# Kernel tuning notes

Hardware: AMD Instinct MI355X
Metric: run time of the kernel (lower is better)

Reference implementation:

```python
import jax, jax.numpy as jnp
import numpy as np

NEG_SLOPE = 0.2
EPS = 1e-16


def gat_conv(x, edge_index, W, att_src, att_dst, bias, heads, out_ch, concat):
    """PyG GATConv (eval mode, add_self_loops=True).
    x: [N, F_in], edge_index: [2, E] with row0=src(j), row1=dst(i).
    W: [F_in, heads*out_ch], att_src/att_dst: [heads, out_ch], bias: [heads*out_ch] or [out_ch].
    """
    N = x.shape[0]
    loop = jnp.arange(N, dtype=edge_index.dtype)
    src = jnp.concatenate([edge_index[0], loop])
    dst = jnp.concatenate([edge_index[1], loop])

    h = (x @ W).reshape(N, heads, out_ch)                 # [N, H, C]
    a_src = jnp.sum(h * att_src[None], axis=-1)           # [N, H]
    a_dst = jnp.sum(h * att_dst[None], axis=-1)           # [N, H]

    alpha = jax.nn.leaky_relu(a_src[src] + a_dst[dst], NEG_SLOPE)  # [E, H]
    # segment softmax over incoming edges of each destination node
    m = jax.ops.segment_max(alpha, dst, num_segments=N)   # [N, H]
    e = jnp.exp(alpha - m[dst])                           # [E, H]
    s = jax.ops.segment_sum(e, dst, num_segments=N)       # [N, H]
    alpha = e / (s[dst] + EPS)                            # [E, H]

    out = jax.ops.segment_sum(h[src] * alpha[:, :, None], dst, num_segments=N)  # [N, H, C]
    if concat:
        out = out.reshape(N, heads * out_ch)
    else:
        out = out.mean(axis=1)
    return out + bias


def setup_inputs() -> dict:
    key = jax.random.key(0)
    ks = jax.random.split(key, 12)
    N, E, F_in, C = 100000, 1600000, 512, 16
    H1, O1 = 8, 8
    hid = H1 * O1  # 64
    sc1 = 1.0 / np.sqrt(F_in)
    sc2 = 1.0 / np.sqrt(hid)
    return {
        "x": jax.random.normal(ks[0], (N, F_in), jnp.float32),
        "edge_index": jax.random.randint(ks[1], (2, E), 0, N, jnp.int64),
        "W1": jax.random.normal(ks[2], (F_in, hid), jnp.float32) * sc1,
        "att_src1": jax.random.normal(ks[3], (H1, O1), jnp.float32) * sc2,
        "att_dst1": jax.random.normal(ks[4], (H1, O1), jnp.float32) * sc2,
        "bias1": jnp.zeros((hid,), jnp.float32),
        "W2": jax.random.normal(ks[5], (hid, C), jnp.float32) * sc2,
        "att_src2": jax.random.normal(ks[6], (1, C), jnp.float32) * 0.25,
        "att_dst2": jax.random.normal(ks[7], (1, C), jnp.float32) * 0.25,
        "bias2": jnp.zeros((C,), jnp.float32),
    }


def reference(x, edge_index, W1, att_src1, att_dst1, bias1, W2, att_src2, att_dst2, bias2):
    h = gat_conv(x, edge_index, W1, att_src1, att_dst1, bias1, heads=8, out_ch=8, concat=True)
    h = jax.nn.elu(h)
    C = W2.shape[1]
    node_embeddings = gat_conv(h, edge_index, W2, att_src2, att_dst2, bias2, heads=1, out_ch=C, concat=True)
    out = jax.nn.softmax(node_embeddings, axis=-1)
    return (out, node_embeddings)
```

## Files before the change

kernel.cpp:

```cpp
#include <hip/hip_runtime.h>
#include <hip/hip_bf16.h>

#define NEG_SLOPE 0.2f
#define EPSF 1e-16f

typedef __attribute__((ext_vector_type(8))) short bf16x8;
typedef __attribute__((ext_vector_type(4))) float f32x4;

__device__ inline unsigned short f2bf(float x) {
  unsigned int u = __float_as_uint(x);
  return (unsigned short)((u + 0x7fffu + ((u >> 16) & 1u)) >> 16);
}
__device__ inline float bf2f(unsigned short h) {
  return __uint_as_float(((unsigned int)h) << 16);
}

__device__ __forceinline__ void gload16(const void* src, void* dst) {
  __builtin_amdgcn_global_load_lds(
      (const __attribute__((address_space(1))) unsigned int*)src,
      (__attribute__((address_space(3))) unsigned int*)dst, 16, 0, 0);
}

__global__ __launch_bounds__(256) void prep_w_kernel(const float* __restrict__ W,
                                                     unsigned short* __restrict__ wb) {
  int idx = blockIdx.x * 256 + threadIdx.x;
  if (idx >= 512 * 64) return;
  int k = idx >> 6, c = idx & 63;
  float w = W[idx];
  unsigned short h = f2bf(w);
  unsigned short l = f2bf(w - bf2f(h));
  int ch = k >> 5, kin = k & 31;
  int Ap = ((c << 6) + (kin << 1)) ^ ((c & 7) << 4);
  wb[ch * 4096 + (Ap >> 1)] = h;
  wb[ch * 4096 + 2048 + (Ap >> 1)] = l;
}

__global__ __launch_bounds__(256) void gemm1_kernel(const float* __restrict__ x,
                                                    const unsigned short* __restrict__ wb,
                                                    const float* __restrict__ atts,
                                                    const float* __restrict__ attd,
                                                    unsigned short* __restrict__ h1b,
                                                    float* __restrict__ a1s,
                                                    float* __restrict__ a1d, int N) {
  __shared__ __align__(16) float As[2][4096];
  __shared__ __align__(16) unsigned short Bs[2][4096];
  const int tid = threadIdx.x, wv = tid >> 6, lane = tid & 63;
  const int row0 = blockIdx.x * 128;

  const float* asrc[4];
  int aldo[4];
#pragma unroll
  for (int i = 0; i < 4; ++i) {
    int u = i * 256 + wv * 64 + lane;
    int row = u >> 3, w = u & 7;
    int rg = row0 + row;
    if (rg >= N) rg = N - 1;
    asrc[i] = x + (size_t)rg * 512 + ((w ^ (row & 7)) << 2);
    aldo[i] = (i * 256 + wv * 64) * 4;
  }
  const unsigned short* bsrc[2];
  int bldo[2];
#pragma unroll
  for (int i = 0; i < 2; ++i) {
    int u = i * 256 + wv * 64 + lane;
    bsrc[i] = wb + (size_t)u * 8;
    bldo[i] = (i * 256 + wv * 64) * 8;
  }

  const int kofs = (lane >> 4) * 8;
  const int cbase = lane & 15;
  int ardo[2][2];
#pragma unroll
  for (int rt = 0; rt < 2; ++rt) {
    int r = wv * 32 + rt * 16 + cbase;
#pragma unroll
    for (int h = 0; h < 2; ++h)
      ardo[rt][h] = r * 32 + ((((kofs >> 2) + h) ^ (r & 7)) << 2);
  }
  int brdo[4];
#pragma unroll
  for (int ct = 0; ct < 4; ++ct) {
    int c = ct * 16 + cbase;
    brdo[ct] = (((c << 6) + (kofs << 1)) ^ ((c & 7) << 4)) >> 1;
  }

  f32x4 acc[2][4] = {};

  auto stage = [&](int b, int ch) {
#pragma unroll
    for (int i = 0; i < 4; ++i) gload16(asrc[i] + ch * 32, &As[b][aldo[i]]);
#pragma unroll
    for (int i = 0; i < 2; ++i) gload16(bsrc[i] + ch * 4096, &Bs[b][bldo[i]]);
  };

  stage(0, 0);
  for (int ch = 0; ch < 16; ++ch) {
    const int b = ch & 1;
    if (ch < 15) {
      stage(b ^ 1, ch + 1);
      asm volatile("s_waitcnt vmcnt(6)" ::: "memory");
    } else {
      asm volatile("s_waitcnt vmcnt(0)" ::: "memory");
    }
    __builtin_amdgcn_s_barrier();
    __builtin_amdgcn_sched_barrier(0);

#pragma unroll
    for (int rt = 0; rt < 2; ++rt) {
      float4 a0 = *(const float4*)(&As[b][ardo[rt][0]]);
      float4 a1 = *(const float4*)(&As[b][ardo[rt][1]]);
      float av[8] = {a0.x, a0.y, a0.z, a0.w, a1.x, a1.y, a1.z, a1.w};
      bf16x8 ah, al;
#pragma unroll
      for (int j = 0; j < 8; ++j) {
        unsigned int u = __float_as_uint(av[j]);
        ah[j] = (short)(unsigned short)(u >> 16);
        float lo = av[j] - __uint_as_float(u & 0xffff0000u);
        al[j] = (short)(unsigned short)(__float_as_uint(lo) >> 16);
      }
#pragma unroll
      for (int ct = 0; ct < 4; ++ct) {
        bf16x8 bh = *(const bf16x8*)(&Bs[b][brdo[ct]]);
        bf16x8 bl = *(const bf16x8*)(&Bs[b][brdo[ct] + 2048]);
        acc[rt][ct] = __builtin_amdgcn_mfma_f32_16x16x32_bf16(ah, bh, acc[rt][ct], 0, 0, 0);
        acc[rt][ct] = __builtin_amdgcn_mfma_f32_16x16x32_bf16(al, bh, acc[rt][ct], 0, 0, 0);
        acc[rt][ct] = __builtin_amdgcn_mfma_f32_16x16x32_bf16(ah, bl, acc[rt][ct], 0, 0, 0);
      }
    }
    asm volatile("s_waitcnt lgkmcnt(0)" ::: "memory");
    __builtin_amdgcn_s_barrier();
  }

  float wS[4], wD[4];
#pragma unroll
  for (int ct = 0; ct < 4; ++ct) {
    wS[ct] = atts[ct * 16 + cbase];
    wD[ct] = attd[ct * 16 + cbase];
  }
#pragma unroll
  for (int rt = 0; rt < 2; ++rt) {
#pragma unroll
    for (int ct = 0; ct < 4; ++ct) {
#pragma unroll
      for (int j = 0; j < 4; ++j) {
        int r = row0 + wv * 32 + rt * 16 + (lane >> 4) * 4 + j;
        float a = acc[rt][ct][j];
        if (r < N) h1b[(size_t)r * 64 + ct * 16 + cbase] = f2bf(a);
        float ps = a * wS[ct], pd = a * wD[ct];
        ps += __shfl_xor(ps, 1); pd += __shfl_xor(pd, 1);
        ps += __shfl_xor(ps, 2); pd += __shfl_xor(pd, 2);
        ps += __shfl_xor(ps, 4); pd += __shfl_xor(pd, 4);
        if ((lane & 7) == 0 && r < N) {
          int h = ct * 2 + ((lane >> 3) & 1);
          a1s[r * 8 + h] = ps;
          a1d[r * 8 + h] = pd;
        }
      }
    }
  }
}

__global__ __launch_bounds__(256) void init_deg_kernel(int* __restrict__ deg, int N) {
  int i = blockIdx.x * 256 + threadIdx.x;
  if (i < N) deg[i] = 1;
}

__global__ __launch_bounds__(256) void count_kernel(const int* __restrict__ ei, int E, int* __restrict__ deg) {
  int e = blockIdx.x * 256 + threadIdx.x;
  if (e < E) atomicAdd(&deg[ei[E + e]], 1);
}

__global__ __launch_bounds__(256) void scan1_kernel(int* __restrict__ data, int* __restrict__ blocksum, int N) {
  __shared__ int wave_tot[4];
  int t = threadIdx.x;
  int base = blockIdx.x * 1024;
  int v[4];
  int sum = 0;
#pragma unroll
  for (int i = 0; i < 4; ++i) {
    int idx = base + t * 4 + i;
    v[i] = sum;
    int d = (idx < N) ? data[idx] : 0;
    sum += d;
  }
  int lane = t & 63, wv = t >> 6;
  int x = sum;
#pragma unroll
  for (int ofs = 1; ofs < 64; ofs <<= 1) {
    int y = __shfl_up(x, ofs);
    if (lane >= ofs) x += y;
  }
  if (lane == 63) wave_tot[wv] = x;
  __syncthreads();
  int wofs = 0;
  for (int w = 0; w < wv; ++w) wofs += wave_tot[w];
  int excl_thread = wofs + x - sum;
#pragma unroll
  for (int i = 0; i < 4; ++i) {
    int idx = base + t * 4 + i;
    if (idx < N) data[idx] = excl_thread + v[i];
  }
  if (t == 255) blocksum[blockIdx.x] = wofs + x;
}

__global__ __launch_bounds__(256) void scan2_kernel(int* __restrict__ blocksum, int nb) {
  __shared__ int sm[256];
  int t = threadIdx.x;
  int x = (t < nb) ? blocksum[t] : 0;
  sm[t] = x;
  __syncthreads();
  for (int ofs = 1; ofs < 256; ofs <<= 1) {
    int y = (t >= ofs) ? sm[t - ofs] : 0;
    __syncthreads();
    sm[t] += y;
    __syncthreads();
  }
  if (t < nb) blocksum[t] = sm[t] - x;
}

__global__ __launch_bounds__(256) void scan3_kernel(const int* __restrict__ excl, const int* __restrict__ blocksum,
                                                    int* __restrict__ rowptr, int* __restrict__ cursor,
                                                    int N, int ET) {
  int idx = blockIdx.x * 256 + threadIdx.x;
  if (idx < N) {
    int r = excl[idx] + blocksum[idx >> 10];
    rowptr[idx] = r;
    cursor[idx] = r;
  }
  if (idx == N) rowptr[N] = ET;
}

__global__ __launch_bounds__(256) void scatter_kernel(const int* __restrict__ ei, int E, int ET,
                                                      int* __restrict__ cursor, int* __restrict__ esrc, int N) {
  const int cls = blockIdx.x & 7;
  const int nlo = (int)(((long long)N * cls) >> 3);
  const int nhi = (int)(((long long)N * (cls + 1)) >> 3);
  const int chunk = blockIdx.x >> 3;
  const int nchunks = gridDim.x >> 3;
  const long long stride = (long long)nchunks * 256;
  for (long long e = (long long)chunk * 256 + threadIdx.x; e < ET; e += stride) {
    int s, d;
    if (e < E) { d = ei[E + e]; s = ei[e]; }
    else       { d = (int)(e - E); s = d; }
    if (d >= nlo && d < nhi) {
      int pos = atomicAdd(&cursor[d], 1);
      esrc[pos] = s;
    }
  }
}

__global__ __launch_bounds__(256) void agg1_kernel(const int* __restrict__ rowptr, const int* __restrict__ esrc,
                                                   const float* __restrict__ a1s, const float* __restrict__ a1d,
                                                   const unsigned short* __restrict__ h1b,
                                                   const float* __restrict__ bias1,
                                                   unsigned short* __restrict__ h2b, int N) {
  const int wid = (blockIdx.x * 256 + threadIdx.x) >> 6;
  const int lane = threadIdx.x & 63;
  const int half = lane >> 5, l = lane & 31;
  const int nA = wid * 2;
  if (nA >= N) return;
  const int n = nA + half;
  const bool nvalid = n < N;
  const int nc = nvalid ? n : nA;
  const int h = l >> 2;
  const int c2 = l * 2;

  const float ad = a1d[(unsigned)nc * 8 + h];
  const int beg = rowptr[nc];
  const int deg = nvalid ? (rowptr[nc + 1] - beg) : 0;
  const int degO = __shfl_xor(deg, 32);
  const int dmax = max(deg, degO);
  const int dcl = max(deg, 1) - 1;

  float acc0 = 0.f, acc1 = 0.f, wsum = 0.f;
  for (int it = 0; it < dmax; it += 2) {
    int k0 = beg + min(it, dcl);
    int k1 = beg + min(it + 1, dcl);
    float m0 = (it < deg) ? 1.f : 0.f;
    float m1 = (it + 1 < deg) ? 1.f : 0.f;
    int s0 = esrc[k0], s1 = esrc[k1];
    unsigned int g0 = *(const unsigned int*)(h1b + ((unsigned)s0 * 64 + c2));
    unsigned int g1 = *(const unsigned int*)(h1b + ((unsigned)s1 * 64 + c2));
    float al0 = a1s[(unsigned)s0 * 8 + h] + ad;
    float al1 = a1s[(unsigned)s1 * 8 + h] + ad;
    al0 = fmaxf(al0, NEG_SLOPE * al0);
    al1 = fmaxf(al1, NEG_SLOPE * al1);
    float w0 = __expf(al0) * m0;
    float w1 = __expf(al1) * m1;
    acc0 = fmaf(w0, bf2f((unsigned short)(g0 & 0xffff)), acc0);
    acc1 = fmaf(w0, bf2f((unsigned short)(g0 >> 16)), acc1);
    acc0 = fmaf(w1, bf2f((unsigned short)(g1 & 0xffff)), acc0);
    acc1 = fmaf(w1, bf2f((unsigned short)(g1 >> 16)), acc1);
    wsum += w0 + w1;
  }
  float inv = 1.f / (wsum + EPSF);
  float2 b2 = *(const float2*)(bias1 + c2);
  float v0 = acc0 * inv + b2.x;
  float v1 = acc1 * inv + b2.y;
  v0 = (v0 > 0.f) ? v0 : expm1f(v0);
  v1 = (v1 > 0.f) ? v1 : expm1f(v1);
  if (nvalid) {
    unsigned int pack = (unsigned int)f2bf(v0) | ((unsigned int)f2bf(v1) << 16);
    *(unsigned int*)(h2b + ((unsigned)n * 64 + c2)) = pack;
  }
}

__global__ __launch_bounds__(256) void l2_proj_kernel(const unsigned short* __restrict__ h2b,
                                                      const float* __restrict__ W2,
                                                      const float* __restrict__ atts, const float* __restrict__ attd,
                                                      unsigned short* __restrict__ gb, float* __restrict__ a2s,
                                                      float* __restrict__ a2d, int N) {
  __shared__ float w[1024];
  int tid = threadIdx.x;
  for (int i = tid; i < 1024; i += 256) w[i] = W2[i];
  __syncthreads();
  int gid = blockIdx.x * 256 + tid;
  int n = gid >> 4, c = gid & 15;
  if (n >= N) return;
  const unsigned short* hr = h2b + (size_t)n * 64;
  float acc = 0.f;
#pragma unroll
  for (int k8 = 0; k8 < 8; ++k8) {
    bf16x8 hv = *(const bf16x8*)(hr + k8 * 8);
#pragma unroll
    for (int j = 0; j < 8; ++j)
      acc = fmaf(bf2f((unsigned short)hv[j]), w[(k8 * 8 + j) * 16 + c], acc);
  }
  gb[(size_t)n * 16 + c] = f2bf(acc);
  float ps = acc * atts[c], pd = acc * attd[c];
#pragma unroll
  for (int m = 1; m < 16; m <<= 1) { ps += __shfl_xor(ps, m); pd += __shfl_xor(pd, m); }
  if (c == 0) { a2s[n] = ps; a2d[n] = pd; }
}

__global__ __launch_bounds__(256) void agg2_kernel(const int* __restrict__ rowptr, const int* __restrict__ esrc,
                                                   const float* __restrict__ a2s, const float* __restrict__ a2d,
                                                   const unsigned short* __restrict__ gb,
                                                   const float* __restrict__ bias2,
                                                   float* __restrict__ out_sm, float* __restrict__ emb, int N) {
  int wid = (blockIdx.x * 256 + threadIdx.x) >> 6;
  int lane = threadIdx.x & 63;
  if (wid >= N) return;
  int n = wid;
  int c = lane & 15, sub = lane >> 4;
  float ad = a2d[n];
  int beg = rowptr[n], end = rowptr[n + 1];
  float acc = 0.f, wsum = 0.f;
  for (int k = beg + sub; k < end; k += 4) {
    int s = esrc[k];
    float al = a2s[s] + ad;
    al = fmaxf(al, NEG_SLOPE * al);
    float w = __expf(al);
    acc = fmaf(w, bf2f(gb[(unsigned)s * 16 + c]), acc);
    wsum += w;
  }
  acc += __shfl_xor(acc, 16); acc += __shfl_xor(acc, 32);
  wsum += __shfl_xor(wsum, 16); wsum += __shfl_xor(wsum, 32);
  float v = acc / (wsum + EPSF) + bias2[c];
  float m = v;
#pragma unroll
  for (int k2 = 1; k2 < 16; k2 <<= 1) m = fmaxf(m, __shfl_xor(m, k2));
  float e = __expf(v - m);
  float ssum = e;
#pragma unroll
  for (int k2 = 1; k2 < 16; k2 <<= 1) ssum += __shfl_xor(ssum, k2);
  if (sub == 0) {
    emb[(size_t)n * 16 + c] = v;
    out_sm[(size_t)n * 16 + c] = e / ssum;
  }
}

extern "C" void kernel_launch(void* const* d_in, const int* in_sizes, int n_in,
                              void* d_out, int out_size, void* d_ws, size_t ws_size,
                              hipStream_t stream) {
  const float* x     = (const float*)d_in[0];
  const int*   ei    = (const int*)d_in[1];
  const float* W1    = (const float*)d_in[2];
  const float* atts1 = (const float*)d_in[3];
  const float* attd1 = (const float*)d_in[4];
  const float* bias1 = (const float*)d_in[5];
  const float* W2    = (const float*)d_in[6];
  const float* atts2 = (const float*)d_in[7];
  const float* attd2 = (const float*)d_in[8];
  const float* bias2 = (const float*)d_in[9];

  const int N = in_sizes[0] / 512;
  const int E = in_sizes[1] / 2;
  const int ET = E + N;

  char* wp = (char*)d_ws;
  unsigned short* h1b = (unsigned short*)wp;        wp += (size_t)N * 64 * 2;
  unsigned short* h2b = (unsigned short*)wp;        wp += (size_t)N * 64 * 2;
  float* a1s = (float*)wp;                          wp += (size_t)N * 8 * 4;
  float* a1d = (float*)wp;                          wp += (size_t)N * 8 * 4;
  unsigned short* gb = (unsigned short*)wp;         wp += (size_t)N * 16 * 2;
  float* a2s = (float*)wp;                          wp += (size_t)N * 4;
  float* a2d = (float*)wp;                          wp += (size_t)N * 4;
  int* deg = (int*)wp;                              wp += (size_t)N * 4;
  int* rowptr = (int*)wp;                           wp += (size_t)(N + 1) * 4;
  int* cursor = (int*)wp;                           wp += (size_t)N * 4;
  int* blocksum = (int*)wp;                         wp += 256 * 4;
  int* esrc = (int*)wp;                             wp += (size_t)ET * 4;
  unsigned short* wb = (unsigned short*)wp;         wp += 512 * 64 * 2 * 2;

  float* out_sm = (float*)d_out;
  float* emb    = out_sm + (size_t)N * 16;

  const int nb = (N + 1023) / 1024;

  init_deg_kernel<<<(N + 255) / 256, 256, 0, stream>>>(deg, N);
  count_kernel<<<(E + 255) / 256, 256, 0, stream>>>(ei, E, deg);
  scan1_kernel<<<nb, 256, 0, stream>>>(deg, blocksum, N);
  scan2_kernel<<<1, 256, 0, stream>>>(blocksum, nb);
  scan3_kernel<<<(N + 256) / 256, 256, 0, stream>>>(deg, blocksum, rowptr, cursor, N, ET);
  scatter_kernel<<<8 * 1024, 256, 0, stream>>>(ei, E, ET, cursor, esrc, N);

  prep_w_kernel<<<128, 256, 0, stream>>>(W1, wb);
  gemm1_kernel<<<(N + 127) / 128, 256, 0, stream>>>(x, wb, atts1, attd1, h1b, a1s, a1d, N);
  agg1_kernel<<<(N + 7) / 8, 256, 0, stream>>>(rowptr, esrc, a1s, a1d, h1b, bias1, h2b, N);

  l2_proj_kernel<<<(N * 16 + 255) / 256, 256, 0, stream>>>(h2b, W2, atts2, attd2, gb, a2s, a2d, N);
  agg2_kernel<<<(N + 3) / 4, 256, 0, stream>>>(rowptr, esrc, a2s, a2d, gb, bias2, out_sm, emb, N);
}
```

Measured before the change: 342.0 us.

## Make gemm1 wave-independent: per-wave A staging, B fragments read directly from global

Rewrites the first-layer GEMM so each wave owns its own 32-row tile and double-buffers only its A slice in LDS. This removes the workgroup-wide barriers. The split-bf16 W matrix is now stored transposed (hi and lo arrays, column-major by output channel), and each lane loads its B fragments straight from global/L2 into registers instead of staging them through LDS. This cuts LDS traffic and lets waves run decoupled, at the cost of more global/L2 loads for B per wave and higher register pressure under launch_bounds(256,4).

```diff
diff --git a/kernel.cpp b/kernel.cpp
--- a/kernel.cpp
+++ b/kernel.cpp
@@ -22,93 +22,80 @@
 }
 
 __global__ __launch_bounds__(256) void prep_w_kernel(const float* __restrict__ W,
-                                                     unsigned short* __restrict__ wb) {
+                                                     unsigned short* __restrict__ wt_hi,
+                                                     unsigned short* __restrict__ wt_lo) {
   int idx = blockIdx.x * 256 + threadIdx.x;
   if (idx >= 512 * 64) return;
   int k = idx >> 6, c = idx & 63;
   float w = W[idx];
   unsigned short h = f2bf(w);
   unsigned short l = f2bf(w - bf2f(h));
-  int ch = k >> 5, kin = k & 31;
-  int Ap = ((c << 6) + (kin << 1)) ^ ((c & 7) << 4);
-  wb[ch * 4096 + (Ap >> 1)] = h;
-  wb[ch * 4096 + 2048 + (Ap >> 1)] = l;
-}
-
-__global__ __launch_bounds__(256) void gemm1_kernel(const float* __restrict__ x,
-                                                    const unsigned short* __restrict__ wb,
-                                                    const float* __restrict__ atts,
-                                                    const float* __restrict__ attd,
-                                                    unsigned short* __restrict__ h1b,
-                                                    float* __restrict__ a1s,
-                                                    float* __restrict__ a1d, int N) {
-  __shared__ __align__(16) float As[2][4096];
-  __shared__ __align__(16) unsigned short Bs[2][4096];
+  wt_hi[c * 512 + k] = h;
+  wt_lo[c * 512 + k] = l;
+}
+
+__global__ __launch_bounds__(256, 4) void gemm1_kernel(const float* __restrict__ x,
+                                                       const unsigned short* __restrict__ wt_hi,
+                                                       const unsigned short* __restrict__ wt_lo,
+                                                       const float* __restrict__ atts,
+                                                       const float* __restrict__ attd,
+                                                       unsigned short* __restrict__ h1b,
+                                                       float* __restrict__ a1s,
+                                                       float* __restrict__ a1d, int N) {
+  __shared__ __align__(16) float As[4][2][1024];
   const int tid = threadIdx.x, wv = tid >> 6, lane = tid & 63;
-  const int row0 = blockIdx.x * 128;
+  const int wtile = blockIdx.x * 4 + wv;
+  const int r0w = wtile * 32;
+  if (r0w >= N) return;
 
   const float* asrc[4];
-  int aldo[4];
 #pragma unroll
   for (int i = 0; i < 4; ++i) {
-    int u = i * 256 + wv * 64 + lane;
-    int row = u >> 3, w = u & 7;
-    int rg = row0 + row;
+    int rg = r0w + i * 8 + (lane >> 3);
     if (rg >= N) rg = N - 1;
-    asrc[i] = x + (size_t)rg * 512 + ((w ^ (row & 7)) << 2);
-    aldo[i] = (i * 256 + wv * 64) * 4;
-  }
-  const unsigned short* bsrc[2];
-  int bldo[2];
-#pragma unroll
-  for (int i = 0; i < 2; ++i) {
-    int u = i * 256 + wv * 64 + lane;
-    bsrc[i] = wb + (size_t)u * 8;
-    bldo[i] = (i * 256 + wv * 64) * 8;
-  }
-
+    asrc[i] = x + (size_t)rg * 512 + (((lane & 7) ^ (lane >> 3)) << 2);
+  }
   const int kofs = (lane >> 4) * 8;
   const int cbase = lane & 15;
   int ardo[2][2];
 #pragma unroll
   for (int rt = 0; rt < 2; ++rt) {
-    int r = wv * 32 + rt * 16 + cbase;
+    int R = rt * 16 + cbase;
+    int s0 = (lane >> 4) * 2;
 #pragma unroll
     for (int h = 0; h < 2; ++h)
-      ardo[rt][h] = r * 32 + ((((kofs >> 2) + h) ^ (r & 7)) << 2);
-  }
-  int brdo[4];
-#pragma unroll
-  for (int ct = 0; ct < 4; ++ct) {
-    int c = ct * 16 + cbase;
-    brdo[ct] = (((c << 6) + (kofs << 1)) ^ ((c & 7) << 4)) >> 1;
-  }
+      ardo[rt][h] = R * 32 + (((s0 + h) ^ (R & 7)) << 2);
+  }
+  const unsigned short* bph = wt_hi + (size_t)cbase * 512 + kofs;
+  const unsigned short* bpl = wt_lo + (size_t)cbase * 512 + kofs;
 
   f32x4 acc[2][4] = {};
 
-  auto stage = [&](int b, int ch) {
-#pragma unroll
-    for (int i = 0; i < 4; ++i) gload16(asrc[i] + ch * 32, &As[b][aldo[i]]);
-#pragma unroll
-    for (int i = 0; i < 2; ++i) gload16(bsrc[i] + ch * 4096, &Bs[b][bldo[i]]);
-  };
-
-  stage(0, 0);
+#pragma unroll
+  for (int i = 0; i < 4; ++i) gload16(asrc[i], &As[wv][0][i * 256]);
+
+#pragma unroll
   for (int ch = 0; ch < 16; ++ch) {
-    const int b = ch & 1;
+    const int buf = ch & 1;
+    bf16x8 bh[4], bl[4];
+#pragma unroll
+    for (int ct = 0; ct < 4; ++ct) {
+      bh[ct] = *(const bf16x8*)(bph + ct * 16 * 512 + ch * 32);
+      bl[ct] = *(const bf16x8*)(bpl + ct * 16 * 512 + ch * 32);
+    }
+    __builtin_amdgcn_sched_barrier(0);
     if (ch < 15) {
-      stage(b ^ 1, ch + 1);
-      asm volatile("s_waitcnt vmcnt(6)" ::: "memory");
+#pragma unroll
+      for (int i = 0; i < 4; ++i) gload16(asrc[i] + (ch + 1) * 32, &As[wv][buf ^ 1][i * 256]);
+      asm volatile("s_waitcnt vmcnt(4)" ::: "memory");
     } else {
       asm volatile("s_waitcnt vmcnt(0)" ::: "memory");
     }
-    __builtin_amdgcn_s_barrier();
     __builtin_amdgcn_sched_barrier(0);
-
 #pragma unroll
     for (int rt = 0; rt < 2; ++rt) {
-      float4 a0 = *(const float4*)(&As[b][ardo[rt][0]]);
-      float4 a1 = *(const float4*)(&As[b][ardo[rt][1]]);
+      float4 a0 = *(const float4*)(&As[wv][buf][ardo[rt][0]]);
+      float4 a1 = *(const float4*)(&As[wv][buf][ardo[rt][1]]);
       float av[8] = {a0.x, a0.y, a0.z, a0.w, a1.x, a1.y, a1.z, a1.w};
       bf16x8 ah, al;
 #pragma unroll
@@ -120,15 +107,11 @@
       }
 #pragma unroll
       for (int ct = 0; ct < 4; ++ct) {
-        bf16x8 bh = *(const bf16x8*)(&Bs[b][brdo[ct]]);
-        bf16x8 bl = *(const bf16x8*)(&Bs[b][brdo[ct] + 2048]);
-        acc[rt][ct] = __builtin_amdgcn_mfma_f32_16x16x32_bf16(ah, bh, acc[rt][ct], 0, 0, 0);
-        acc[rt][ct] = __builtin_amdgcn_mfma_f32_16x16x32_bf16(al, bh, acc[rt][ct], 0, 0, 0);
-        acc[rt][ct] = __builtin_amdgcn_mfma_f32_16x16x32_bf16(ah, bl, acc[rt][ct], 0, 0, 0);
+        acc[rt][ct] = __builtin_amdgcn_mfma_f32_16x16x32_bf16(ah, bh[ct], acc[rt][ct], 0, 0, 0);
+        acc[rt][ct] = __builtin_amdgcn_mfma_f32_16x16x32_bf16(al, bh[ct], acc[rt][ct], 0, 0, 0);
+        acc[rt][ct] = __builtin_amdgcn_mfma_f32_16x16x32_bf16(ah, bl[ct], acc[rt][ct], 0, 0, 0);
       }
     }
-    asm volatile("s_waitcnt lgkmcnt(0)" ::: "memory");
-    __builtin_amdgcn_s_barrier();
   }
 
   float wS[4], wD[4];
@@ -143,7 +126,7 @@
     for (int ct = 0; ct < 4; ++ct) {
 #pragma unroll
       for (int j = 0; j < 4; ++j) {
-        int r = row0 + wv * 32 + rt * 16 + (lane >> 4) * 4 + j;
+        int r = r0w + rt * 16 + (lane >> 4) * 4 + j;
         float a = acc[rt][ct][j];
         if (r < N) h1b[(size_t)r * 64 + ct * 16 + cbase] = f2bf(a);
         float ps = a * wS[ct], pd = a * wD[ct];
@@ -401,7 +384,8 @@
   int* cursor = (int*)wp;                           wp += (size_t)N * 4;
   int* blocksum = (int*)wp;                         wp += 256 * 4;
   int* esrc = (int*)wp;                             wp += (size_t)ET * 4;
-  unsigned short* wb = (unsigned short*)wp;         wp += 512 * 64 * 2 * 2;
+  unsigned short* wt_hi = (unsigned short*)wp;      wp += 512 * 64 * 2;
+  unsigned short* wt_lo = (unsigned short*)wp;      wp += 512 * 64 * 2;
 
   float* out_sm = (float*)d_out;
   float* emb    = out_sm + (size_t)N * 16;
@@ -415,8 +399,11 @@
   scan3_kernel<<<(N + 256) / 256, 256, 0, stream>>>(deg, blocksum, rowptr, cursor, N, ET);
   scatter_kernel<<<8 * 1024, 256, 0, stream>>>(ei, E, ET, cursor, esrc, N);
 
-  prep_w_kernel<<<128, 256, 0, stream>>>(W1, wb);
-  gemm1_kernel<<<(N + 127) / 128, 256, 0, stream>>>(x, wb, atts1, attd1, h1b, a1s, a1d, N);
+  prep_w_kernel<<<128, 256, 0, stream>>>(W1, wt_hi, wt_lo);
+  {
+    int ntiles = (N + 31) / 32;
+    gemm1_kernel<<<(ntiles + 3) / 4, 256, 0, stream>>>(x, wt_hi, wt_lo, atts1, attd1, h1b, a1s, a1d, N);
+  }
   agg1_kernel<<<(N + 7) / 8, 256, 0, stream>>>(rowptr, esrc, a1s, a1d, h1b, bias1, h2b, N);
 
   l2_proj_kernel<<<(N * 16 + 255) / 256, 256, 0, stream>>>(h2b, W2, atts2, attd2, gb, a2s, a2d, N);
```

After: 370.9 us. +8.4%, slower.
